# Optimization experiments

Hardware: AMD Instinct MI355X
Metric: run time of the kernel (lower is better)

The kernel has to match this reference:

```python
import jax, jax.numpy as jnp
import numpy as np
from math import log, sqrt

B, L, D, H, NL = 2, 2048, 512, 8, 4
HD = D // H
BOUND = 1.0 / sqrt(5.0)  # NormalizationLayer init bound


def setup_inputs() -> dict:
    key = jax.random.key(0)
    ks = jax.random.split(key, 12)
    s = 1.0 / sqrt(D)
    return {
        "base": jax.random.normal(ks[0], (B, L, D), jnp.float32),
        "qkv_w": jax.random.normal(ks[1], (NL, 3 * D, D), jnp.float32) * s,
        "qkv_b": jax.random.normal(ks[2], (NL, 3 * D), jnp.float32) * 0.01,
        "f1_w": jax.random.normal(ks[3], (NL, D, D), jnp.float32) * s,
        "f1_b": jax.random.normal(ks[4], (NL, D), jnp.float32) * 0.01,
        "f2_w": jax.random.normal(ks[5], (NL, D, D), jnp.float32) * s,
        "f2_b": jax.random.normal(ks[6], (NL, D), jnp.float32) * 0.01,
        "n1_scale": jax.random.uniform(ks[7], (NL,), jnp.float32, -BOUND, BOUND),
        "n1_bias": jax.random.uniform(ks[8], (NL,), jnp.float32, -BOUND, BOUND),
        "n2_scale": jax.random.uniform(ks[9], (NL,), jnp.float32, -BOUND, BOUND),
        "n2_bias": jax.random.uniform(ks[10], (NL,), jnp.float32, -BOUND, BOUND),
    }


def _timing_signal(seq_dim, model_dim, seq_start=1):
    # seq_len=None path of timing_signal_1d
    nt = model_dim // 2
    inc = log(10000.0) / max(nt - 1, 1)
    inv = jnp.exp(jnp.arange(nt, dtype=jnp.float32) * (-inc))  # [nt]
    pos = jnp.arange(-seq_start, seq_dim - seq_start, dtype=jnp.float32)[:, None]  # [L,1]
    st = pos * inv[None, :]  # [L, nt]
    return jnp.concatenate([jnp.sin(st), jnp.cos(st)], axis=1)[None]  # [1, L, D]


def _norm(x, scale, bias):
    # mean/std over dims (1,2), scalar affine
    m = jnp.mean(x, axis=(1, 2), keepdims=True)
    sd = jnp.sqrt(jnp.mean((x - m) ** 2, axis=(1, 2), keepdims=True))
    return (x - m) / sd * scale + bias


def reference(base, qkv_w, qkv_b, f1_w, f1_b, f2_w, f2_b,
              n1_scale, n1_bias, n2_scale, n2_bias):
    x = base + _timing_signal(L, D).astype(base.dtype)
    for i in range(NL):
        qkv = x @ qkv_w[i].T + qkv_b[i]  # [B,L,3D]
        q, k, v = jnp.split(qkv, 3, axis=2)
        q = q.reshape(B, L, H, HD)
        k = k.reshape(B, L, H, HD)
        v = v.reshape(B, L, H, HD)
        a = jnp.einsum('blhd,bmhd->bhlm', q, k) / sqrt(HD)  # [B,H,L,L]
        a = jax.nn.softmax(a, axis=-1)
        o = jnp.einsum('bhlm,bmhd->blhd', a, v).reshape(B, L, D)
        h = _norm(o @ f1_w[i].T + f1_b[i] + x, n1_scale[i], n1_bias[i])
        x = _norm(jax.nn.relu(h @ f2_w[i].T + f2_b[i]) + h, n2_scale[i], n2_bias[i])
    return x
```

## Files before the change

kernel.cpp:

```cpp
#include <hip/hip_runtime.h>
#include <hip/hip_bf16.h>

#define DEV __device__ __forceinline__

typedef __attribute__((ext_vector_type(8))) short bf16x8;
typedef __attribute__((ext_vector_type(4))) float f32x4;
typedef __attribute__((ext_vector_type(16))) float f32x16;
typedef __attribute__((ext_vector_type(4))) unsigned short u16x4;
typedef __attribute__((ext_vector_type(8))) unsigned short u16x8;


DEV unsigned short f2bf(float f) {
  union { float f; unsigned u; } v; v.f = f;
  unsigned r = v.u + 0x7FFFu + ((v.u >> 16) & 1u);
  return (unsigned short)(r >> 16);
}

DEV float bf2f(unsigned short u) {
  union { unsigned u; float f; } v; v.u = ((unsigned)u) << 16; return v.f;
}

DEV void gload_lds16(const void* g, void* lds) {
  __builtin_amdgcn_global_load_lds(
      (const __attribute__((address_space(1))) unsigned int*)g,
      (__attribute__((address_space(3))) unsigned int*)lds, 16, 0, 0);
}

DEV int swz128(int r, int cb) { return r * 128 + (cb ^ ((r & 7) << 4)); }

__global__ __launch_bounds__(256) void cvt_kernel(const float* __restrict__ s,
                                                  unsigned short* __restrict__ d, int n4) {
  int i = blockIdx.x * 256 + threadIdx.x;
  if (i >= n4) return;
  float4 v = ((const float4*)s)[i];
  u16x4 r; r[0] = f2bf(v.x); r[1] = f2bf(v.y); r[2] = f2bf(v.z); r[3] = f2bf(v.w);
  ((u16x4*)d)[i] = r;
}

__global__ __launch_bounds__(256) void rowsum_kernel(const unsigned short* __restrict__ w,
                                                     float* __restrict__ rs) {
  int row = blockIdx.x * 4 + (threadIdx.x >> 6);
  int lane = threadIdx.x & 63;
  u16x8 v = *(const u16x8*)&w[(size_t)row * 512 + lane * 8];
  float s = 0.f;
#pragma unroll
  for (int e = 0; e < 8; ++e) s += bf2f(v[e]);
#pragma unroll
  for (int m = 1; m < 64; m <<= 1) s += __shfl_xor(s, m);
  if (lane == 0) rs[row] = s;
}

__global__ __launch_bounds__(256) void init_x_kernel(const float* __restrict__ base,
                                                     float* __restrict__ xf,
                                                     unsigned short* __restrict__ xb) {
  int i = blockIdx.x * 256 + threadIdx.x;
  int d = i & 511;
  int l = (i >> 9) & 2047;
  const float NEG_INC = -(float)(9.210340371976184 / 255.0);
  int j = d & 255;
  float w = expf((float)j * NEG_INC);
  float ang = (float)(l - 1) * w;
  float ts = (d < 256) ? sinf(ang) : cosf(ang);
  float v = base[i] + ts;
  xf[i] = v;
  xb[i] = f2bf(v);
}

DEV void norm_affine(const float* pin, int batch, const float* nsc, const float* nbi,
                     int nlayer, int lane, float& a_in, float& bi_in) {
  const float* p = pin + batch * 1024;
  float s = 0.f, s2 = 0.f;
#pragma unroll
  for (int k = 0; k < 8; ++k) {
    int idx = lane + 64 * k;
    s += p[2 * idx];
    s2 += p[2 * idx + 1];
  }
#pragma unroll
  for (int m = 1; m < 64; m <<= 1) { s += __shfl_xor(s, m); s2 += __shfl_xor(s2, m); }
  const float invn = 1.f / 1048576.f;
  float mean = s * invn;
  float var = s2 * invn - mean * mean;
  float aa = nsc[nlayer] / sqrtf(var);
  a_in = aa;
  bi_in = nbi[nlayer] - mean * aa;
}

template<int MODE, int BM, int BN, int WR, int WC>
__global__ __launch_bounds__(WR * WC * 64) void gemm_kernel(
    const unsigned short* __restrict__ A,
    const unsigned short* __restrict__ W,
    const float* __restrict__ bias,
    const float* __restrict__ resid,
    unsigned short* __restrict__ outb,
    unsigned short* __restrict__ vtout,
    float* __restrict__ outf,
    float* __restrict__ partials,
    const float* __restrict__ pin,
    const float* __restrict__ nsc,
    const float* __restrict__ nbi,
    int nlayer,
    const float* __restrict__ rs,
    int N) {
  constexpr int T = WR * WC * 64;
  constexpr int WTM = BM / WR, WTN = BN / WC;
  constexpr int MR = WTM / 16, NR = WTN / 16;
  constexpr int IA = BM * 8 / T, IB = BN * 8 / T;
  static_assert(IA + IB == 6, "vmcnt immediate assumes 6 loads per stage");
  __shared__ __align__(16) unsigned short Al[3][BM * 64];
  __shared__ __align__(16) unsigned short Bl[3][BN * 64];
  __shared__ float red[WR * WC * 2];
  const int tid = threadIdx.x;
  const int lane = tid & 63, wid = tid >> 6;
  const int wr = wid / WC, wc = wid % WC;
  const int m0 = blockIdx.y * BM, n0 = blockIdx.x * BN;
  const int batch = m0 >> 11;

  float a_in = 1.f, bi_in = 0.f;
  if (pin) norm_affine(pin, batch, nsc, nbi, nlayer, lane, a_in, bi_in);
  asm volatile("s_waitcnt vmcnt(0)" ::: "memory");

  auto stage = [&](int kt, int buf) {
#pragma unroll
    for (int it = 0; it < IA; ++it) {
      int c = it * T + tid;
      int row = c >> 3, sub = c & 7;
      gload_lds16((const char*)A + (m0 + row) * 1024 + kt * 128 + sub * 16,
                  (char*)Al[buf] + (it * T + wid * 64) * 16);
    }
#pragma unroll
    for (int it = 0; it < IB; ++it) {
      int c = it * T + tid;
      int row = c >> 3, sub = c & 7;
      gload_lds16((const char*)W + (n0 + row) * 1024 + kt * 128 + sub * 16,
                  (char*)Bl[buf] + (it * T + wid * 64) * 16);
    }
  };

  f32x4 acc[MR][NR];
#pragma unroll
  for (int m = 0; m < MR; ++m)
#pragma unroll
    for (int n = 0; n < NR; ++n) acc[m][n] = (f32x4){0.f, 0.f, 0.f, 0.f};

  stage(0, 0);
  for (int kt = 0; kt < 8; ++kt) {
    int cur = kt % 3;
    if (kt < 7) {
      stage(kt + 1, (kt + 1) % 3);
      asm volatile("s_waitcnt vmcnt(6)" ::: "memory");
    } else {
      asm volatile("s_waitcnt vmcnt(0)" ::: "memory");
    }
    __builtin_amdgcn_s_barrier();
    asm volatile("" ::: "memory");
#pragma unroll
    for (int ks = 0; ks < 2; ++ks) {
      bf16x8 af[MR], bfr[NR];
#pragma unroll
      for (int m = 0; m < MR; ++m)
        af[m] = *(const bf16x8*)&Al[cur][(wr * WTM + m * 16 + (lane & 15)) * 64 + ks * 32 + (lane >> 4) * 8];
#pragma unroll
      for (int n = 0; n < NR; ++n)
        bfr[n] = *(const bf16x8*)&Bl[cur][(wc * WTN + n * 16 + (lane & 15)) * 64 + ks * 32 + (lane >> 4) * 8];
      __builtin_amdgcn_s_setprio(1);
#pragma unroll
      for (int m = 0; m < MR; ++m)
#pragma unroll
        for (int n = 0; n < NR; ++n)
          acc[m][n] = __builtin_amdgcn_mfma_f32_16x16x32_bf16(af[m], bfr[n], acc[m][n], 0, 0, 0);
      __builtin_amdgcn_s_setprio(0);
    }
  }

  float ps = 0.f, ps2 = 0.f;
#pragma unroll
  for (int m = 0; m < MR; ++m) {
    int row = m0 + wr * WTM + m * 16 + ((lane >> 4) << 2);
#pragma unroll
    for (int n = 0; n < NR; ++n) {
      int col = n0 + wc * WTN + n * 16 + (lane & 15);
      float bv = bias[col];
      float rsv = (MODE == 1) ? 0.f : rs[col];
      if (MODE == 0) {
        u16x4 q4;
#pragma unroll
        for (int j = 0; j < 4; ++j) {
          float v = a_in * acc[m][n][j] + bi_in * rsv + bv;
          if (col < 512) v *= 0.180336880f;
          unsigned short bf = f2bf(v);
          q4[j] = bf;
          outb[(row + j) * N + col] = bf;
        }
        if (col >= 1024) {
          int c2 = col - 1024;
          size_t va = ((size_t)((row >> 11) * 8 + (c2 >> 6)) * 64 + (c2 & 63)) * 2048 + (row & 2047);
          *(u16x4*)&vtout[va] = q4;
        }
      } else {
#pragma unroll
        for (int j = 0; j < 4; ++j) {
          int idx = (row + j) * N + col;
          float v;
          if (MODE == 1) {
            v = acc[m][n][j] + bv + (a_in * resid[idx] + bi_in);
          } else {
            v = fmaxf(a_in * acc[m][n][j] + bi_in * rsv + bv, 0.f) +
                (a_in * resid[idx] + bi_in);
          }
          outf[idx] = v;
          outb[idx] = f2bf(v);
          ps += v; ps2 += v * v;
        }
      }
    }
  }
  if (MODE != 0) {
#pragma unroll
    for (int s = 1; s < 64; s <<= 1) {
      ps += __shfl_xor(ps, s);
      ps2 += __shfl_xor(ps2, s);
    }
    if (lane == 0) { red[wid * 2] = ps; red[wid * 2 + 1] = ps2; }
    __syncthreads();
    if (tid == 0) {
      float s = 0.f, s2 = 0.f;
#pragma unroll
      for (int w = 0; w < WR * WC; ++w) { s += red[w * 2]; s2 += red[w * 2 + 1]; }
      constexpr int YPB = 2048 / BM;
      int slot = (blockIdx.y % YPB) * gridDim.x + blockIdx.x;
      partials[(batch * 512 + slot) * 2] = s;
      partials[(batch * 512 + slot) * 2 + 1] = s2;
    }
  }
}

__global__ __launch_bounds__(256) void attn_kernel(
    const unsigned short* __restrict__ qkv,
    const unsigned short* __restrict__ vT,
    unsigned short* __restrict__ op0,
    unsigned short* __restrict__ op1,
    unsigned short* __restrict__ op2,
    float* __restrict__ ssums) {
  __shared__ __align__(16) unsigned short Kl[3][64 * 64];
  __shared__ __align__(16) unsigned short Vl[3][64 * 64];
  const int tid = threadIdx.x;
  const int lane = tid & 63, wid = tid >> 6;
  const int lq = lane & 31;
  const int g = lane >> 5;
  const int lin = blockIdx.x;
  const int grp = lin % 48;
  const int xq = lin / 48;
  const int bh = grp / 3, sp = grp % 3;
  const int b = bh >> 3, h = bh & 7;
  const int nt = (sp == 2) ? 10 : 11;
  const int t0 = sp * 11;
  const int l0 = xq * 128;
  const int qrow = l0 + wid * 32 + lq;

  const size_t qoff = (size_t)b * 2048 * 1536 + h * 64;
  const size_t koff = qoff + 512;
  const size_t voff = (size_t)(b * 8 + h) * 64 * 2048;

  bf16x8 qf[4];
#pragma unroll
  for (int dm = 0; dm < 4; ++dm)
    qf[dm] = *(const bf16x8*)&qkv[qoff + (size_t)qrow * 1536 + dm * 16 + g * 8];

  auto stageKV = [&](int t, int buf) {
#pragma unroll
    for (int it = 0; it < 2; ++it) {
      int c = it * 256 + tid;
      int row = c >> 3, sub = c & 7;
      int sw = (sub * 16) ^ ((row & 7) << 4);
      gload_lds16((const char*)qkv + (koff + (size_t)(t * 64 + row) * 1536) * 2 + sw,
                  (char*)Kl[buf] + (it * 256 + wid * 64) * 16);
    }
#pragma unroll
    for (int it = 0; it < 2; ++it) {
      int c = it * 256 + tid;
      int row = c >> 3, sub = c & 7;
      int sw = (sub * 16) ^ ((row & 7) << 4);
      gload_lds16((const char*)vT + (voff + (size_t)row * 2048 + t * 64) * 2 + sw,
                  (char*)Vl[buf] + (it * 256 + wid * 64) * 16);
    }
  };

  union { unsigned short su[8]; bf16x8 v; } ou;
#pragma unroll
  for (int j = 0; j < 8; ++j) ou.su[j] = 0x3F80;
  const bf16x8 onesf = ou.v;

  f32x16 oacc[2], sacc;
#pragma unroll
  for (int i = 0; i < 16; ++i) { oacc[0][i] = 0.f; oacc[1][i] = 0.f; sacc[i] = 0.f; }

  auto pack2 = [&](const float* p, bf16x8& paA, bf16x8& paB) {
    unsigned w[8];
#pragma unroll
    for (int j = 0; j < 8; ++j)
      asm("v_cvt_pk_bf16_f32 %0, %1, %2" : "=v"(w[j]) : "v"(p[2 * j]), "v"(p[2 * j + 1]));
    asm("v_permlane32_swap_b32 %0, %1" : "+v"(w[0]), "+v"(w[2]));
    asm("v_permlane32_swap_b32 %0, %1" : "+v"(w[1]), "+v"(w[3]));
    asm("v_permlane32_swap_b32 %0, %1" : "+v"(w[4]), "+v"(w[6]));
    asm("v_permlane32_swap_b32 %0, %1" : "+v"(w[5]), "+v"(w[7]));
    union { unsigned u[4]; bf16x8 v; } a, c;
    a.u[0] = w[2]; a.u[1] = w[3]; a.u[2] = w[0]; a.u[3] = w[1];
    c.u[0] = w[6]; c.u[1] = w[7]; c.u[2] = w[4]; c.u[3] = w[5];
    paA = a.v; paB = c.v;
  };

  stageKV(t0, 0);
  for (int tt = 0; tt < nt; ++tt) {
    int cur = tt % 3;
    if (tt < nt - 1) {
      stageKV(t0 + tt + 1, (tt + 1) % 3);
      asm volatile("s_waitcnt vmcnt(4)" ::: "memory");
    } else {
      asm volatile("s_waitcnt vmcnt(0)" ::: "memory");
    }
    __builtin_amdgcn_s_barrier();
    asm volatile("" ::: "memory");

    f32x16 s0, s1;
#pragma unroll
    for (int i = 0; i < 16; ++i) { s0[i] = 0.f; s1[i] = 0.f; }
#pragma unroll
    for (int dm = 0; dm < 4; ++dm) {
      bf16x8 kf0 = *(const bf16x8*)((const char*)Kl[cur] + swz128(lq, dm * 32 + g * 16));
      bf16x8 kf1 = *(const bf16x8*)((const char*)Kl[cur] + swz128(32 + lq, dm * 32 + g * 16));
      __builtin_amdgcn_s_setprio(1);
      s0 = __builtin_amdgcn_mfma_f32_32x32x16_bf16(kf0, qf[dm], s0, 0, 0, 0);
      s1 = __builtin_amdgcn_mfma_f32_32x32x16_bf16(kf1, qf[dm], s1, 0, 0, 0);
      __builtin_amdgcn_s_setprio(0);
    }

    float p0[16], p1[16];
#pragma unroll
    for (int i = 0; i < 16; ++i) {
      p0[i] = __builtin_amdgcn_exp2f(s0[i]);
      p1[i] = __builtin_amdgcn_exp2f(s1[i]);
    }

    bf16x8 fr[4];
    pack2(p0, fr[0], fr[1]);
    pack2(p1, fr[2], fr[3]);

    __builtin_amdgcn_s_setprio(1);
#pragma unroll
    for (int q = 0; q < 4; ++q)
      sacc = __builtin_amdgcn_mfma_f32_32x32x16_bf16(onesf, fr[q], sacc, 0, 0, 0);
    __builtin_amdgcn_s_setprio(0);

#pragma unroll
    for (int dn = 0; dn < 2; ++dn) {
      bf16x8 vf[4];
#pragma unroll
      for (int q = 0; q < 4; ++q)
        vf[q] = *(const bf16x8*)((const char*)Vl[cur] +
                                 swz128(dn * 32 + lq, q * 32 + (g ^ 1) * 16));
      __builtin_amdgcn_s_setprio(1);
#pragma unroll
      for (int q = 0; q < 4; ++q)
        oacc[dn] = __builtin_amdgcn_mfma_f32_32x32x16_bf16(vf[q], fr[q], oacc[dn], 0, 0, 0);
      __builtin_amdgcn_s_setprio(0);
    }
  }

  unsigned short* op = (sp == 0) ? op0 : (sp == 1) ? op1 : op2;
  size_t obase = (size_t)bh * 131072;
#pragma unroll
  for (int dn = 0; dn < 2; ++dn)
#pragma unroll
    for (int ro = 0; ro < 4; ++ro) {
      int d0 = dn * 32 + ro * 8 + g * 4;
      u16x4 o4;
#pragma unroll
      for (int e = 0; e < 4; ++e) o4[e] = f2bf(oacc[dn][ro * 4 + e]);
      *(u16x4*)&op[obase + (size_t)qrow * 64 + d0] = o4;
    }
  if (lane < 32)
    ssums[(size_t)sp * 32768 + (size_t)bh * 2048 + qrow] = sacc[0];
}

__global__ __launch_bounds__(256) void attn_combine_kernel(
    const unsigned short* __restrict__ op0,
    const unsigned short* __restrict__ op1,
    const unsigned short* __restrict__ op2,
    const float* __restrict__ ssums,
    unsigned short* __restrict__ o) {
  const int tid = threadIdx.x;
  int row = blockIdx.x * 16 + (tid >> 4);
  int c0 = (tid & 15) * 4;
  float inv = 1.f / (ssums[row] + ssums[32768 + row] + ssums[65536 + row]);
  u16x4 a0 = *(const u16x4*)&op0[(size_t)row * 64 + c0];
  u16x4 a1 = *(const u16x4*)&op1[(size_t)row * 64 + c0];
  u16x4 a2 = *(const u16x4*)&op2[(size_t)row * 64 + c0];
  int bh = row >> 11, l = row & 2047;
  int b = bh >> 3, h = bh & 7;
  u16x4 r;
#pragma unroll
  for (int e = 0; e < 4; ++e)
    r[e] = f2bf((bf2f(a0[e]) + bf2f(a1[e]) + bf2f(a2[e])) * inv);
  *(u16x4*)&o[((size_t)(b * 2048 + l)) * 512 + h * 64 + c0] = r;
}

__global__ __launch_bounds__(256) void faffine_kernel(
    const float* __restrict__ in,
    const float* __restrict__ pin,
    const float* __restrict__ nsc,
    const float* __restrict__ nbi,
    int nlayer,
    float* __restrict__ out) {
  int i4 = blockIdx.x * 256 + threadIdx.x;
  size_t i = (size_t)i4 * 4;
  int batch = (int)(i >> 20);
  int lane = threadIdx.x & 63;
  float a, bi;
  norm_affine(pin, batch, nsc, nbi, nlayer, lane, a, bi);
  float4 v = *(const float4*)(in + i);
  float4 r;
  r.x = v.x * a + bi; r.y = v.y * a + bi; r.z = v.z * a + bi; r.w = v.w * a + bi;
  *(float4*)(out + i) = r;
}

extern "C" void kernel_launch(void* const* d_in, const int* in_sizes, int n_in,
                              void* d_out, int out_size, void* d_ws, size_t ws_size,
                              hipStream_t stream) {
  (void)in_sizes; (void)n_in; (void)out_size; (void)ws_size;
  const float* base  = (const float*)d_in[0];
  const float* qkv_w = (const float*)d_in[1];
  const float* qkv_b = (const float*)d_in[2];
  const float* f1_w  = (const float*)d_in[3];
  const float* f1_b  = (const float*)d_in[4];
  const float* f2_w  = (const float*)d_in[5];
  const float* f2_b  = (const float*)d_in[6];
  const float* n1s   = (const float*)d_in[7];
  const float* n1b   = (const float*)d_in[8];
  const float* n2s   = (const float*)d_in[9];
  const float* n2b   = (const float*)d_in[10];

  char* ws = (char*)d_ws;
  float*          t2_f32 = (float*)(ws + 0);
  unsigned short* t2_bf  = (unsigned short*)(ws + (8u << 20));
  unsigned short* op2    = (unsigned short*)(ws + (8u << 20));
  unsigned short* qkv_bf = (unsigned short*)(ws + (12u << 20));
  unsigned short* o_bf   = (unsigned short*)(ws + (12u << 20));
  unsigned short* t1_bf  = (unsigned short*)(ws + (16u << 20));
  unsigned short* vT     = (unsigned short*)(ws + (28u << 20));
  float*          ssums  = (float*)(ws + (32u << 20));
  float*          t1_f32 = (float*)(ws + (28u << 20));
  unsigned short* op0    = (unsigned short*)(ws + (36u << 20));
  unsigned short* op1    = (unsigned short*)(ws + (40u << 20));
  unsigned short* wq     = (unsigned short*)(ws + (44u << 20));
  unsigned short* w1     = (unsigned short*)(ws + (50u << 20));
  unsigned short* w2     = (unsigned short*)(ws + (52u << 20));
  float*          parts1 = (float*)(ws + (54u << 20));
  float*          parts2 = (float*)(ws + (54u << 20) + 16384);
  float*          rsq    = (float*)(ws + (54u << 20) + 32768);
  float*          rs2    = (float*)(ws + (54u << 20) + 65536);

  cvt_kernel<<<3072, 256, 0, stream>>>(qkv_w, wq, 786432);
  cvt_kernel<<<1024, 256, 0, stream>>>(f1_w, w1, 262144);
  cvt_kernel<<<1024, 256, 0, stream>>>(f2_w, w2, 262144);
  rowsum_kernel<<<1536, 256, 0, stream>>>(wq, rsq);
  rowsum_kernel<<<512, 256, 0, stream>>>(w2, rs2);
  init_x_kernel<<<8192, 256, 0, stream>>>(base, t2_f32, t2_bf);

  for (int L = 0; L < 4; ++L) {
    const float* pin_in = (L == 0) ? nullptr : parts2;
    gemm_kernel<0, 64, 128, 1, 4><<<dim3(12, 64), 256, 0, stream>>>(
        t2_bf, wq + L * 786432, qkv_b + L * 1536, nullptr, qkv_bf, vT, nullptr,
        nullptr, pin_in, n2s, n2b, L - 1, rsq + L * 1536, 1536);
    attn_kernel<<<768, 256, 0, stream>>>(qkv_bf, vT, op0, op1, op2, ssums);
    attn_combine_kernel<<<2048, 256, 0, stream>>>(op0, op1, op2, ssums, o_bf);
    gemm_kernel<1, 32, 64, 1, 2><<<dim3(8, 128), 128, 0, stream>>>(
        o_bf, w1 + L * 262144, f1_b + L * 512, t2_f32, t1_bf, nullptr, t1_f32,
        parts1, pin_in, n2s, n2b, L - 1, nullptr, 512);
    gemm_kernel<2, 32, 64, 1, 2><<<dim3(8, 128), 128, 0, stream>>>(
        t1_bf, w2 + L * 262144, f2_b + L * 512, t1_f32, t2_bf, nullptr, t2_f32,
        parts2, parts1, n1s, n1b, L, rs2 + L * 512, 512);
  }
  faffine_kernel<<<2048, 256, 0, stream>>>(t2_f32, parts2, n2s, n2b, 3, (float*)d_out);
}
```

Measured before the change: 344.7 us.

## Split attention keys four ways and load V straight into registers

The attention kernel now splits the key range into four chunks of 8 tiles instead of three uneven chunks, raising the grid from 768 to 1024 blocks. A fourth partial-output buffer and partial-sum slot are added, and the combine kernel sums four partials. V fragments are now read directly from global memory into registers each iteration instead of being staged through LDS. This halves LDS use and adds an occupancy hint of 3 blocks per unit. The trade-offs are more combine traffic, uncoalesced-style per-lane global V loads, and K-tile readiness that now relies on compiler-inserted waits rather than explicit vmcnt waits.

```diff
diff --git a/kernel.cpp b/kernel.cpp
--- a/kernel.cpp
+++ b/kernel.cpp
@@ -235,39 +235,39 @@
   }
 }
 
-__global__ __launch_bounds__(256) void attn_kernel(
+__global__ __launch_bounds__(256, 3) void attn_kernel(
     const unsigned short* __restrict__ qkv,
     const unsigned short* __restrict__ vT,
     unsigned short* __restrict__ op0,
     unsigned short* __restrict__ op1,
     unsigned short* __restrict__ op2,
+    unsigned short* __restrict__ op3,
     float* __restrict__ ssums) {
   __shared__ __align__(16) unsigned short Kl[3][64 * 64];
-  __shared__ __align__(16) unsigned short Vl[3][64 * 64];
   const int tid = threadIdx.x;
   const int lane = tid & 63, wid = tid >> 6;
   const int lq = lane & 31;
   const int g = lane >> 5;
+  const int gx = g ^ 1;
   const int lin = blockIdx.x;
-  const int grp = lin % 48;
-  const int xq = lin / 48;
-  const int bh = grp / 3, sp = grp % 3;
+  const int grp = lin & 63;
+  const int xq = lin >> 6;
+  const int bh = grp >> 2, sp = grp & 3;
   const int b = bh >> 3, h = bh & 7;
-  const int nt = (sp == 2) ? 10 : 11;
-  const int t0 = sp * 11;
+  const int t0 = sp * 8;
   const int l0 = xq * 128;
   const int qrow = l0 + wid * 32 + lq;
 
   const size_t qoff = (size_t)b * 2048 * 1536 + h * 64;
   const size_t koff = qoff + 512;
-  const size_t voff = (size_t)(b * 8 + h) * 64 * 2048;
+  const unsigned short* vbase = vT + (size_t)(b * 8 + h) * 64 * 2048 + (size_t)lq * 2048 + gx * 8;
 
   bf16x8 qf[4];
 #pragma unroll
   for (int dm = 0; dm < 4; ++dm)
     qf[dm] = *(const bf16x8*)&qkv[qoff + (size_t)qrow * 1536 + dm * 16 + g * 8];
 
-  auto stageKV = [&](int t, int buf) {
+  auto stageK = [&](int t, int buf) {
 #pragma unroll
     for (int it = 0; it < 2; ++it) {
       int c = it * 256 + tid;
@@ -275,14 +275,6 @@
       int sw = (sub * 16) ^ ((row & 7) << 4);
       gload_lds16((const char*)qkv + (koff + (size_t)(t * 64 + row) * 1536) * 2 + sw,
                   (char*)Kl[buf] + (it * 256 + wid * 64) * 16);
-    }
-#pragma unroll
-    for (int it = 0; it < 2; ++it) {
-      int c = it * 256 + tid;
-      int row = c >> 3, sub = c & 7;
-      int sw = (sub * 16) ^ ((row & 7) << 4);
-      gload_lds16((const char*)vT + (voff + (size_t)row * 2048 + t * 64) * 2 + sw,
-                  (char*)Vl[buf] + (it * 256 + wid * 64) * 16);
     }
   };
 
@@ -310,17 +302,21 @@
     paA = a.v; paB = c.v;
   };
 
-  stageKV(t0, 0);
-  for (int tt = 0; tt < nt; ++tt) {
+  stageK(t0, 0);
+  asm volatile("s_waitcnt vmcnt(0)" ::: "memory");
+  for (int tt = 0; tt < 8; ++tt) {
     int cur = tt % 3;
-    if (tt < nt - 1) {
-      stageKV(t0 + tt + 1, (tt + 1) % 3);
-      asm volatile("s_waitcnt vmcnt(4)" ::: "memory");
-    } else {
-      asm volatile("s_waitcnt vmcnt(0)" ::: "memory");
-    }
+    if (tt < 7) stageK(t0 + tt + 1, (tt + 1) % 3);
     __builtin_amdgcn_s_barrier();
     asm volatile("" ::: "memory");
+
+    const int kv0 = (t0 + tt) * 64;
+    bf16x8 vf[2][4];
+#pragma unroll
+    for (int dn = 0; dn < 2; ++dn)
+#pragma unroll
+      for (int q = 0; q < 4; ++q)
+        vf[dn][q] = *(const bf16x8*)(vbase + (size_t)dn * 32 * 2048 + kv0 + q * 16);
 
     f32x16 s0, s1;
 #pragma unroll
@@ -350,24 +346,15 @@
 #pragma unroll
     for (int q = 0; q < 4; ++q)
       sacc = __builtin_amdgcn_mfma_f32_32x32x16_bf16(onesf, fr[q], sacc, 0, 0, 0);
+#pragma unroll
+    for (int dn = 0; dn < 2; ++dn)
+#pragma unroll
+      for (int q = 0; q < 4; ++q)
+        oacc[dn] = __builtin_amdgcn_mfma_f32_32x32x16_bf16(vf[dn][q], fr[q], oacc[dn], 0, 0, 0);
     __builtin_amdgcn_s_setprio(0);
-
-#pragma unroll
-    for (int dn = 0; dn < 2; ++dn) {
-      bf16x8 vf[4];
-#pragma unroll
-      for (int q = 0; q < 4; ++q)
-        vf[q] = *(const bf16x8*)((const char*)Vl[cur] +
-                                 swz128(dn * 32 + lq, q * 32 + (g ^ 1) * 16));
-      __builtin_amdgcn_s_setprio(1);
-#pragma unroll
-      for (int q = 0; q < 4; ++q)
-        oacc[dn] = __builtin_amdgcn_mfma_f32_32x32x16_bf16(vf[q], fr[q], oacc[dn], 0, 0, 0);
-      __builtin_amdgcn_s_setprio(0);
-    }
-  }
-
-  unsigned short* op = (sp == 0) ? op0 : (sp == 1) ? op1 : op2;
+  }
+
+  unsigned short* op = (sp == 0) ? op0 : (sp == 1) ? op1 : (sp == 2) ? op2 : op3;
   size_t obase = (size_t)bh * 131072;
 #pragma unroll
   for (int dn = 0; dn < 2; ++dn)
@@ -387,21 +374,23 @@
     const unsigned short* __restrict__ op0,
     const unsigned short* __restrict__ op1,
     const unsigned short* __restrict__ op2,
+    const unsigned short* __restrict__ op3,
     const float* __restrict__ ssums,
     unsigned short* __restrict__ o) {
   const int tid = threadIdx.x;
   int row = blockIdx.x * 16 + (tid >> 4);
   int c0 = (tid & 15) * 4;
-  float inv = 1.f / (ssums[row] + ssums[32768 + row] + ssums[65536 + row]);
+  float inv = 1.f / (ssums[row] + ssums[32768 + row] + ssums[65536 + row] + ssums[98304 + row]);
   u16x4 a0 = *(const u16x4*)&op0[(size_t)row * 64 + c0];
   u16x4 a1 = *(const u16x4*)&op1[(size_t)row * 64 + c0];
   u16x4 a2 = *(const u16x4*)&op2[(size_t)row * 64 + c0];
+  u16x4 a3 = *(const u16x4*)&op3[(size_t)row * 64 + c0];
   int bh = row >> 11, l = row & 2047;
   int b = bh >> 3, h = bh & 7;
   u16x4 r;
 #pragma unroll
   for (int e = 0; e < 4; ++e)
-    r[e] = f2bf((bf2f(a0[e]) + bf2f(a1[e]) + bf2f(a2[e])) * inv);
+    r[e] = f2bf(((bf2f(a0[e]) + bf2f(a1[e])) + (bf2f(a2[e]) + bf2f(a3[e]))) * inv);
   *(u16x4*)&o[((size_t)(b * 2048 + l)) * 512 + h * 64 + c0] = r;
 }
 
@@ -447,6 +436,7 @@
   unsigned short* qkv_bf = (unsigned short*)(ws + (12u << 20));
   unsigned short* o_bf   = (unsigned short*)(ws + (12u << 20));
   unsigned short* t1_bf  = (unsigned short*)(ws + (16u << 20));
+  unsigned short* op3    = (unsigned short*)(ws + (24u << 20));
   unsigned short* vT     = (unsigned short*)(ws + (28u << 20));
   float*          ssums  = (float*)(ws + (32u << 20));
   float*          t1_f32 = (float*)(ws + (28u << 20));
@@ -472,8 +462,8 @@
     gemm_kernel<0, 64, 128, 1, 4><<<dim3(12, 64), 256, 0, stream>>>(
         t2_bf, wq + L * 786432, qkv_b + L * 1536, nullptr, qkv_bf, vT, nullptr,
         nullptr, pin_in, n2s, n2b, L - 1, rsq + L * 1536, 1536);
-    attn_kernel<<<768, 256, 0, stream>>>(qkv_bf, vT, op0, op1, op2, ssums);
-    attn_combine_kernel<<<2048, 256, 0, stream>>>(op0, op1, op2, ssums, o_bf);
+    attn_kernel<<<1024, 256, 0, stream>>>(qkv_bf, vT, op0, op1, op2, op3, ssums);
+    attn_combine_kernel<<<2048, 256, 0, stream>>>(op0, op1, op2, op3, ssums, o_bf);
     gemm_kernel<1, 32, 64, 1, 2><<<dim3(8, 128), 128, 0, stream>>>(
         o_bf, w1 + L * 262144, f1_b + L * 512, t2_f32, t1_bf, nullptr, t1_f32,
         parts1, pin_in, n2s, n2b, L - 1, nullptr, 512);
```

Measured after the change: 408.1 us. 1.18x slower.
